# Optimization experiments

Hardware: AMD Instinct MI355X
Metric: run time of the kernel (lower is better)

## Reference

```python
import jax, jax.numpy as jnp
import numpy as np

EPS = 1e-10  # faithful quirk: masked scores are set to eps, NOT -inf
LN_EPS = 1e-5
N_HEADS, D_MODEL, D_HEAD, D_MLP = 16, 1024, 64, 4096
INIT_RANGE = 0.02


def setup_inputs() -> dict:
    key = jax.random.key(0)
    ks = jax.random.split(key, 8)
    B, S = 2, 2048
    inp = {
        'residual': jax.random.normal(ks[0], (B, S, D_MODEL), jnp.float32),
        'W_key': jax.random.normal(ks[1], (N_HEADS, D_MODEL, D_HEAD), jnp.float32) * INIT_RANGE,
        'W_query': jax.random.normal(ks[2], (N_HEADS, D_MODEL, D_HEAD), jnp.float32) * INIT_RANGE,
        'W_values': jax.random.normal(ks[3], (N_HEADS, D_MODEL, D_HEAD), jnp.float32) * INIT_RANGE,
        'W_attn_out': jax.random.normal(ks[4], (N_HEADS, D_HEAD, D_MODEL), jnp.float32) * INIT_RANGE,
        'B_key': jnp.zeros((N_HEADS, D_HEAD), jnp.float32),
        'B_query': jnp.zeros((N_HEADS, D_HEAD), jnp.float32),
        'B_values': jnp.zeros((N_HEADS, D_HEAD), jnp.float32),
        'B_attn_out': jnp.zeros((D_MODEL,), jnp.float32),
        'ln1_w': jnp.ones((D_MODEL,), jnp.float32),
        'ln1_b': jnp.zeros((D_MODEL,), jnp.float32),
        'ln2_w': jnp.ones((D_MODEL,), jnp.float32),
        'ln2_b': jnp.zeros((D_MODEL,), jnp.float32),
        'W_mlp_in': jax.random.normal(ks[5], (D_MODEL, D_MLP), jnp.float32) * INIT_RANGE,
        'W_mlp_out': jax.random.normal(ks[6], (D_MLP, D_MODEL), jnp.float32) * INIT_RANGE,
        'B_mlp_in': jnp.zeros((D_MLP,), jnp.float32),
        'B_mlp_out': jnp.zeros((D_MODEL,), jnp.float32),
    }
    return inp


def _layernorm(x, w, b):
    mean = jnp.mean(x, axis=-1, keepdims=True)
    var = jnp.mean(jnp.square(x - mean), axis=-1, keepdims=True)  # biased var
    return (x - mean) / jnp.sqrt(var + LN_EPS) * w + b


def _attention(x, W_key, W_query, W_values, W_attn_out,
               B_key, B_query, B_values, B_attn_out):
    S = x.shape[1]
    keys = jnp.einsum('bse,neh->bsnh', x, W_key) + B_key
    queries = jnp.einsum('bse,neh->bsnh', x, W_query) + B_query
    values = jnp.einsum('bse,neh->bsnh', x, W_values) + B_values
    scores = jnp.einsum('bknh,bqnh->bnqk', keys, queries) / (D_HEAD ** 0.5)
    # faithful to source: positions where query < key are set to eps (not -inf)
    q_idx = jnp.arange(S)[:, None]
    k_idx = jnp.arange(S)[None, :]
    scores = jnp.where(q_idx < k_idx, EPS, scores)
    probs = jax.nn.softmax(scores, axis=3)
    weighted = jnp.einsum('bnqk,bknh->bqnh', probs, values)
    out = jnp.einsum('bqnh,nhe->bqe', weighted, W_attn_out) + B_attn_out
    return out


def reference(residual, W_key, W_query, W_values, W_attn_out,
              B_key, B_query, B_values, B_attn_out,
              ln1_w, ln1_b, ln2_w, ln2_b,
              W_mlp_in, W_mlp_out, B_mlp_in, B_mlp_out):
    mid = _attention(_layernorm(residual, ln1_w, ln1_b),
                     W_key, W_query, W_values, W_attn_out,
                     B_key, B_query, B_values, B_attn_out) + residual
    h = jnp.einsum('bse,em->bsm', _layernorm(mid, ln2_w, ln2_b), W_mlp_in) + B_mlp_in
    h = jax.nn.gelu(h, approximate=False)  # torch nn.GELU default = exact erf
    out = jnp.einsum('bsm,me->bse', h, W_mlp_out) + B_mlp_out + mid
    return out
```

## Files before the change

### kernel.cpp

```cpp
#include <hip/hip_runtime.h>
#include <hip/hip_bf16.h>


typedef __hip_bfloat16 bf16;
typedef __bf16 bf16x8 __attribute__((ext_vector_type(8)));
typedef float f32x4 __attribute__((ext_vector_type(4)));
typedef unsigned short u16x8 __attribute__((ext_vector_type(8)));
#define DEV static __device__ __forceinline__

DEV float b2f(bf16 v) { return __bfloat162float(v); }
DEV bf16 f2b(float v) { return __float2bfloat16(v); }
DEV unsigned short f2bu(float v) { return __builtin_bit_cast(unsigned short, __float2bfloat16(v)); }
DEV float ldin(const void* p, size_t i, int f32) {
  return f32 ? ((const float*)p)[i] : b2f(((const bf16*)p)[i]);
}
DEV void stout(void* p, size_t i, int f32, float v) {
  if (f32) ((float*)p)[i] = v;
  else     ((bf16*)p)[i] = f2b(v);
}
DEV f32x4 mfma16(bf16x8 a, bf16x8 b, f32x4 c) {
  return __builtin_amdgcn_mfma_f32_16x16x32_bf16(a, b, c, 0, 0, 0);
}
DEV float exp2fast(float x) {
  float r;
  asm volatile("v_exp_f32 %0, %1\n\ts_nop 0" : "=v"(r) : "v"(x));
  return r;
}
DEV void gload16(const void* g, void* l) {
  __builtin_amdgcn_global_load_lds(
      (const __attribute__((address_space(1))) unsigned int*)g,
      (__attribute__((address_space(3))) unsigned int*)l, 16, 0, 0);
}

__global__ void detect_kernel(const void* __restrict__ ln1w, int* __restrict__ flag) {
  if (threadIdx.x == 0 && blockIdx.x == 0) {
    const unsigned short* u = (const unsigned short*)ln1w;
    flag[0] = (u[0] == 0x3F80u) ? 0 : 1;
  }
}

__global__ void pack_bias(const void* __restrict__ Bq, const void* __restrict__ Bk,
                          const void* __restrict__ Bv, const void* __restrict__ Bao,
                          const void* __restrict__ Bmi, const void* __restrict__ Bmo,
                          const int* __restrict__ flagp, float* __restrict__ out) {
  int t = blockIdx.x * 256 + threadIdx.x;
  if (t >= 9216) return;
  int f32 = flagp[0];
  float v;
  if (t < 1024)      v = ldin(Bq, t, f32);
  else if (t < 2048) v = ldin(Bk, t - 1024, f32);
  else if (t < 3072) v = ldin(Bv, t - 2048, f32);
  else if (t < 4096) v = ldin(Bao, t - 3072, f32);
  else if (t < 8192) v = ldin(Bmi, t - 4096, f32);
  else               v = ldin(Bmo, t - 8192, f32);
  out[t] = v;
}

__global__ __launch_bounds__(256) void tsplit(const void* __restrict__ src,
                                              bf16* __restrict__ hi,
                                              const int* __restrict__ flagp,
                                              int K, int N) {
  int i = blockIdx.x * 256 + threadIdx.x;
  int f32 = flagp[0];
  int k = i / N, n = i - k * N;
  float v = ldin(src, i, f32);
  hi[(size_t)n * K + k] = f2b(v);
}

__global__ __launch_bounds__(256) void tsplit_qkv(const void* __restrict__ Wq,
                                                  const void* __restrict__ Wk,
                                                  const void* __restrict__ Wv,
                                                  bf16* __restrict__ hi,
                                                  const int* __restrict__ flagp) {
  int i = blockIdx.x * 256 + threadIdx.x;
  int f32 = flagp[0];
  int sec = i >> 20;
  int rem = i & 1048575;
  int hh = rem >> 16, kr = rem & 65535;
  int k = kr >> 6, d = kr & 63;
  const void* W = (sec == 0) ? Wq : (sec == 1) ? Wk : Wv;
  float v = ldin(W, (size_t)hh * 65536 + (size_t)k * 64 + d, f32);
  int n = sec * 1024 + hh * 64 + d;
  hi[(size_t)n * 1024 + k] = f2b(v);
}

__global__ __launch_bounds__(256) void vsuffix(const bf16* __restrict__ v2,
                                               float* __restrict__ suf) {
  const int head = blockIdx.x >> 6, d = blockIdx.x & 63;
  const int t = threadIdx.x;
  const int T = t >> 3, s0 = (t & 7) * 8;
  const bf16* src = v2 + (size_t)head * 131072 + (size_t)T * 4096 + d * 64 + s0;
  u16x8 u = *(const u16x8*)src;
  float s = 0.f;
#pragma unroll
  for (int j = 0; j < 8; j++) s += b2f(__builtin_bit_cast(bf16, (unsigned short)u[j]));
#pragma unroll
  for (int off = 1; off < 8; off <<= 1) s += __shfl_xor(s, off);
  __shared__ float cs[32];
  if ((t & 7) == 0) cs[T] = s;
  __syncthreads();
  if (t < 33) {
    float acc = 0.f;
    for (int j = t; j < 32; j++) acc += cs[j];
    suf[((size_t)head * 33 + t) * 64 + d] = acc;
  }
}

__global__ __launch_bounds__(256) void ln_kernel(const void* __restrict__ x,
                                                 const void* __restrict__ w,
                                                 const void* __restrict__ bb,
                                                 bf16* __restrict__ out,
                                                 const int* __restrict__ flagp) {
  const int f32 = flagp[0];
  const int row = blockIdx.x, t = threadIdx.x;
  const size_t base = (size_t)row * 1024;
  float v[4];
#pragma unroll
  for (int i = 0; i < 4; i++) v[i] = ldin(x, base + t + 256 * i, f32);
  float s1 = v[0] + v[1] + v[2] + v[3];
  float s2 = v[0] * v[0] + v[1] * v[1] + v[2] * v[2] + v[3] * v[3];
#pragma unroll
  for (int off = 32; off; off >>= 1) {
    s1 += __shfl_xor(s1, off);
    s2 += __shfl_xor(s2, off);
  }
  __shared__ float r1[4], r2[4];
  if ((t & 63) == 0) { r1[t >> 6] = s1; r2[t >> 6] = s2; }
  __syncthreads();
  s1 = r1[0] + r1[1] + r1[2] + r1[3];
  s2 = r2[0] + r2[1] + r2[2] + r2[3];
  float mean = s1 * (1.f / 1024.f);
  float var = s2 * (1.f / 1024.f) - mean * mean;
  float rstd = rsqrtf(var + 1e-5f);
#pragma unroll
  for (int i = 0; i < 4; i++) {
    int idx = t + 256 * i;
    out[base + idx] = f2b((v[i] - mean) * rstd * ldin(w, idx, f32) + ldin(bb, idx, f32));
  }
}

template <int MODE>
__global__ __launch_bounds__(256) void gemm_bt2(const bf16* __restrict__ A,
                                                const bf16* __restrict__ BT,
                                                const float* __restrict__ bias,
                                                const void* extra, void* outp,
                                                const int* __restrict__ flagp,
                                                int N, int K, int nx) {
  __shared__ __align__(16) unsigned short As[128][64];
  __shared__ __align__(16) unsigned short Bs[128][64];
  const int f32 = flagp[0];
  const int t = threadIdx.x;
  const int lane = t & 63, wv = t >> 6;
  const int quad = lane >> 4, l15 = lane & 15;
  const int wm = (wv >> 1) * 64, wn = (wv & 1) * 64;
  const int pB = blockIdx.x, cpx = gridDim.x >> 3;
  const int id = (pB & 7) * cpx + (pB >> 3);
  const int m0 = (id / nx) * 128, n0 = (id % nx) * 128;
  f32x4 acc[4][4] = {};
  const int rl = lane >> 3, G = lane & 7;
  const int sg = (G ^ rl) * 8;
  const int l7 = l15 & 7;
  for (int k0 = 0; k0 < K; k0 += 64) {
#pragma unroll
    for (int c = 0; c < 4; c++) {
      const int ch = wv * 4 + c;
      const int row = ch * 8 + rl;
      gload16(A + (size_t)(m0 + row) * K + k0 + sg, &As[ch * 8][0]);
      gload16(BT + (size_t)(n0 + row) * K + k0 + sg, &Bs[ch * 8][0]);
    }
    __syncthreads();
#pragma unroll
    for (int sub = 0; sub < 2; sub++) {
      const int gsw = (((sub * 4 + quad) ^ l7)) * 8;
      bf16x8 af[4], bh[4];
#pragma unroll
      for (int f = 0; f < 4; f++) {
        af[f] = __builtin_bit_cast(bf16x8, *(const u16x8*)&As[wm + f * 16 + l15][gsw]);
        bh[f] = __builtin_bit_cast(bf16x8, *(const u16x8*)&Bs[wn + f * 16 + l15][gsw]);
      }
#pragma unroll
      for (int fm = 0; fm < 4; fm++)
#pragma unroll
        for (int fn = 0; fn < 4; fn++)
          acc[fm][fn] = mfma16(af[fm], bh[fn], acc[fm][fn]);
    }
    __syncthreads();
  }
  if (MODE == 3) {
    bf16* q2 = (bf16*)outp;
    bf16* k2 = q2 + 4194304;
    bf16* v2 = (bf16*)const_cast<void*>(extra);
#pragma unroll
    for (int fm = 0; fm < 4; fm++) {
      int rowb = m0 + wm + fm * 16 + quad * 4;
      int bq = rowb >> 11, sb = rowb & 2047;
#pragma unroll
      for (int fn = 0; fn < 4; fn++) {
        int col = n0 + wn + fn * 16 + l15;
        float bcol = bias[col];
        int sec = col >> 10;
        int hd = col & 1023;
        size_t hbase = (size_t)(bq * 16 + (hd >> 6)) * 131072;
        int d = hd & 63;
        if (sec == 2) {
          unsigned long long pk = 0;
#pragma unroll
          for (int r = 0; r < 4; r++)
            pk |= (unsigned long long)f2bu(acc[fm][fn][r] + bcol) << (16 * r);
          *(unsigned long long*)&v2[hbase + (size_t)(sb >> 6) * 4096 + d * 64 + (sb & 63)] = pk;
        } else {
          bf16* dst = sec ? k2 : q2;
#pragma unroll
          for (int r = 0; r < 4; r++)
            dst[hbase + (size_t)(sb + r) * 64 + d] = f2b(acc[fm][fn][r] + bcol);
        }
      }
    }
  } else {
#pragma unroll
    for (int fm = 0; fm < 4; fm++) {
#pragma unroll
      for (int r = 0; r < 4; r++) {
        int row = m0 + wm + fm * 16 + quad * 4 + r;
#pragma unroll
        for (int fn = 0; fn < 4; fn++) {
          int col = n0 + wn + fn * 16 + l15;
          float v = acc[fm][fn][r] + bias[col];
          if (MODE == 1) {
            size_t idx = (size_t)row * N + col;
            v += ldin(extra, idx, f32);
            stout(outp, idx, f32, v);
          } else {
            v = 0.5f * v * (1.f + erff(v * 0.70710678118654752f));
            ((bf16*)outp)[(size_t)row * N + col] = f2b(v);
          }
        }
      }
    }
  }
}

__global__ __launch_bounds__(256) void gemm_bt3(const bf16* __restrict__ A,
                                                const bf16* __restrict__ BT,
                                                const float* __restrict__ bias,
                                                const void* extra, void* outp,
                                                const int* __restrict__ flagp,
                                                int N, int K) {
  __shared__ __align__(16) unsigned short As[64][64];
  __shared__ __align__(16) unsigned short Bs[128][64];
  const int f32 = flagp[0];
  const int t = threadIdx.x;
  const int lane = t & 63, wv = t >> 6;
  const int quad = lane >> 4, l15 = lane & 15;
  const int wm = (wv >> 1) * 32, wn = (wv & 1) * 64;
  const int pB = blockIdx.x, cpx = gridDim.x >> 3;
  const int id = (pB & 7) * cpx + (pB >> 3);
  const int m0 = (id >> 3) * 64, n0 = (id & 7) * 128;
  f32x4 acc[2][4] = {};
  const int rl = lane >> 3, G = lane & 7;
  const int sg = (G ^ rl) * 8;
  const int l7 = l15 & 7;
  for (int k0 = 0; k0 < K; k0 += 64) {
#pragma unroll
    for (int c = 0; c < 2; c++) {
      const int ch = wv * 2 + c;
      gload16(A + (size_t)(m0 + ch * 8 + rl) * K + k0 + sg, &As[ch * 8][0]);
    }
#pragma unroll
    for (int c = 0; c < 4; c++) {
      const int ch = wv * 4 + c;
      gload16(BT + (size_t)(n0 + ch * 8 + rl) * K + k0 + sg, &Bs[ch * 8][0]);
    }
    __syncthreads();
#pragma unroll
    for (int sub = 0; sub < 2; sub++) {
      const int gsw = (((sub * 4 + quad) ^ l7)) * 8;
      bf16x8 af[2], bh[4];
#pragma unroll
      for (int f = 0; f < 2; f++)
        af[f] = __builtin_bit_cast(bf16x8, *(const u16x8*)&As[wm + f * 16 + l15][gsw]);
#pragma unroll
      for (int f = 0; f < 4; f++)
        bh[f] = __builtin_bit_cast(bf16x8, *(const u16x8*)&Bs[wn + f * 16 + l15][gsw]);
#pragma unroll
      for (int fm = 0; fm < 2; fm++)
#pragma unroll
        for (int fn = 0; fn < 4; fn++)
          acc[fm][fn] = mfma16(af[fm], bh[fn], acc[fm][fn]);
    }
    __syncthreads();
  }
#pragma unroll
  for (int fm = 0; fm < 2; fm++) {
#pragma unroll
    for (int r = 0; r < 4; r++) {
      int row = m0 + wm + fm * 16 + quad * 4 + r;
#pragma unroll
      for (int fn = 0; fn < 4; fn++) {
        int col = n0 + wn + fn * 16 + l15;
        float v = acc[fm][fn][r] + bias[col];
        size_t idx = (size_t)row * N + col;
        v += ldin(extra, idx, f32);
        stout(outp, idx, f32, v);
      }
    }
  }
}

template <int MODE, int QKV>
__global__ __launch_bounds__(256) void gemm_nn(const bf16* __restrict__ A,
                                               const void* __restrict__ B0,
                                               const void* __restrict__ B1,
                                               const void* __restrict__ B2,
                                               const float* __restrict__ bias,
                                               const void* extra, void* outp,
                                               const int* __restrict__ flagp,
                                               int N, int K, size_t ooff) {
  __shared__ unsigned short As[128][40];
  __shared__ unsigned short Bh[128][40];
  __shared__ unsigned short Bl[128][40];
  const int f32 = flagp[0];
  const int t = threadIdx.x;
  const int lane = t & 63, wv = t >> 6;
  const int quad = lane >> 4, l15 = lane & 15;
  const int wm = (wv >> 1) * 64, wn = (wv & 1) * 64;
  const int m0 = blockIdx.y * 128, n0 = blockIdx.x * 128;
  const void* B = B0;
  if (QKV) B = (n0 < 1024) ? B0 : (n0 < 2048) ? B1 : B2;
  f32x4 acc[4][4] = {};
  const int row_a = t >> 2;
  const int kc = (t & 3) * 8;
  const int cB = t & 127;
  const int e0 = t >> 7;
  for (int k0 = 0; k0 < K; k0 += 32) {
    uint4 a0 = *(const uint4*)(A + (size_t)(m0 + row_a) * K + k0 + kc);
    uint4 a1 = *(const uint4*)(A + (size_t)(m0 + 64 + row_a) * K + k0 + kc);
    *(uint4*)&As[row_a][kc] = a0;
    *(uint4*)&As[64 + row_a][kc] = a1;
#pragma unroll
    for (int rep = 0; rep < 8; rep++) {
      int e = (rep * 2 + e0) * 2;
      size_t a0i, a1i;
      if (QKV) {
        int cs = (n0 + cB) & 1023;
        size_t wb = (size_t)(cs >> 6) * 65536 + (cs & 63);
        a0i = wb + (size_t)(k0 + e) * 64;
        a1i = wb + (size_t)(k0 + e + 1) * 64;
      } else {
        a0i = (size_t)(k0 + e) * N + n0 + cB;
        a1i = a0i + N;
      }
      float v0 = ldin(B, a0i, f32);
      float v1 = ldin(B, a1i, f32);
      unsigned short h0 = f2bu(v0), h1 = f2bu(v1);
      float l0 = v0 - b2f(__builtin_bit_cast(bf16, h0));
      float l1 = v1 - b2f(__builtin_bit_cast(bf16, h1));
      *(unsigned int*)&Bh[cB][e] = (unsigned int)h0 | ((unsigned int)h1 << 16);
      *(unsigned int*)&Bl[cB][e] = (unsigned int)f2bu(l0) | ((unsigned int)f2bu(l1) << 16);
    }
    __syncthreads();
    bf16x8 af[4], bh[4], bl[4];
#pragma unroll
    for (int f = 0; f < 4; f++) {
      af[f] = __builtin_bit_cast(bf16x8, *(const u16x8*)&As[wm + f * 16 + l15][quad * 8]);
      bh[f] = __builtin_bit_cast(bf16x8, *(const u16x8*)&Bh[wn + f * 16 + l15][quad * 8]);
      bl[f] = __builtin_bit_cast(bf16x8, *(const u16x8*)&Bl[wn + f * 16 + l15][quad * 8]);
    }
#pragma unroll
    for (int fm = 0; fm < 4; fm++)
#pragma unroll
      for (int fn = 0; fn < 4; fn++)
        acc[fm][fn] = mfma16(af[fm], bh[fn], acc[fm][fn]);
    if (f32) {
#pragma unroll
      for (int fm = 0; fm < 4; fm++)
#pragma unroll
        for (int fn = 0; fn < 4; fn++)
          acc[fm][fn] = mfma16(af[fm], bl[fn], acc[fm][fn]);
    }
    __syncthreads();
  }
#pragma unroll
  for (int fm = 0; fm < 4; fm++) {
#pragma unroll
    for (int r = 0; r < 4; r++) {
      int row = m0 + wm + fm * 16 + quad * 4 + r;
#pragma unroll
      for (int fn = 0; fn < 4; fn++) {
        int col = n0 + wn + fn * 16 + l15;
        float v = acc[fm][fn][r] + bias[col];
        size_t idx = (size_t)row * N + col;
        if (MODE == 1) {
          v += ldin(extra, ooff + idx, f32);
          stout(outp, ooff + idx, f32, v);
        } else if (MODE == 2) {
          v = 0.5f * v * (1.f + erff(v * 0.70710678118654752f));
          ((bf16*)outp)[idx] = f2b(v);
        } else {
          ((bf16*)outp)[idx] = f2b(v);
        }
      }
    }
  }
}

__global__ __launch_bounds__(256, 2) void attn_split(const bf16* __restrict__ qkv2,
                                                     const float* __restrict__ suf,
                                                     float* __restrict__ part0,
                                                     float* __restrict__ part1,
                                                     float* __restrict__ lp0buf,
                                                     float* __restrict__ lp1buf,
                                                     bf16* __restrict__ weighted) {
  __shared__ __align__(16) unsigned short P[4][4][16][72];
  const int t = threadIdx.x;
  const int lane = t & 63, wv = t >> 6;
  const int quad = lane >> 4, l15 = lane & 15;
  const int w = blockIdx.x * 4 + wv;
  const int g = w & 31;
  const int wi = w >> 5;
  int qc, Tlo, Thi, mode;
  if (wi < 32) {
    qc = 31 - (wi >> 1);
    if ((wi & 1) == 0) { Tlo = 0; Thi = 15; mode = 1; }
    else               { Tlo = 16; Thi = qc; mode = 2; }
  } else {
    qc = 47 - wi; Tlo = 0; Thi = qc; mode = 0;
  }
  const int b = g >> 4, n = g & 15;
  const bf16* Qh = qkv2 + (size_t)g * 131072;
  const bf16* Kh = qkv2 + 4194304 + (size_t)g * 131072;
  const bf16* Vh = qkv2 + 8388608 + (size_t)g * 131072;
  bf16x8 aq[4][2];
#pragma unroll
  for (int qg = 0; qg < 4; qg++) {
    size_t qr = (size_t)(qc * 64 + qg * 16 + l15) * 64;
    aq[qg][0] = __builtin_bit_cast(bf16x8, *(const u16x8*)(Qh + qr + quad * 8));
    aq[qg][1] = __builtin_bit_cast(bf16x8, *(const u16x8*)(Qh + qr + 32 + quad * 8));
  }
  float lp[4][4] = {};
  f32x4 o[4][4] = {};
  const float C = 0.125f * 1.44269504088896f;
  for (int T = Tlo; T <= Thi; ++T) {
    const int kk = T * 64;
    u16x8 uk[4][2];
#pragma unroll
    for (int sub = 0; sub < 4; sub++) {
      size_t kr = (size_t)(kk + sub * 16 + l15) * 64;
      uk[sub][0] = *(const u16x8*)(Kh + kr + quad * 8);
      uk[sub][1] = *(const u16x8*)(Kh + kr + 32 + quad * 8);
    }
    const bf16* Vt = Vh + (size_t)T * 4096;
    u16x8 vu[2][4];
#pragma unroll
    for (int sl = 0; sl < 2; sl++)
#pragma unroll
      for (int f = 0; f < 4; f++)
        vu[sl][f] = *(const u16x8*)(Vt + (size_t)(f * 16 + l15) * 64 + sl * 32 + quad * 8);
#pragma unroll
    for (int qg = 0; qg < 4; qg++) {
      const int qgb = qc * 64 + qg * 16 + quad * 4;
      f32x4 s[4];
      __builtin_amdgcn_s_setprio(1);
#pragma unroll
      for (int sub = 0; sub < 4; sub++) {
        f32x4 sc = {0.f, 0.f, 0.f, 0.f};
        sc = mfma16(aq[qg][0], __builtin_bit_cast(bf16x8, uk[sub][0]), sc);
        sc = mfma16(aq[qg][1], __builtin_bit_cast(bf16x8, uk[sub][1]), sc);
        s[sub] = sc;
      }
      __builtin_amdgcn_s_setprio(0);
#pragma unroll
      for (int sub = 0; sub < 4; sub++) {
#pragma unroll
        for (int r = 0; r < 4; r++) {
          float pv = exp2fast(s[sub][r] * C);
          int kg = kk + sub * 16 + l15;
          pv = (qgb + r < kg) ? 1.0f : pv;
          lp[qg][r] += pv;
          P[wv][qg][quad * 4 + r][l15 + 16 * sub] = f2bu(pv);
        }
      }
      u16x8 pu0 = *(const u16x8*)&P[wv][qg][l15][quad * 8];
      u16x8 pu1 = *(const u16x8*)&P[wv][qg][l15][32 + quad * 8];
      __builtin_amdgcn_s_setprio(1);
#pragma unroll
      for (int f = 0; f < 4; f++) {
        o[qg][f] = mfma16(__builtin_bit_cast(bf16x8, pu0), __builtin_bit_cast(bf16x8, vu[0][f]), o[qg][f]);
        o[qg][f] = mfma16(__builtin_bit_cast(bf16x8, pu1), __builtin_bit_cast(bf16x8, vu[1][f]), o[qg][f]);
      }
      __builtin_amdgcn_s_setprio(0);
    }
  }
  if (mode != 1) {
    const float* sp = suf + ((size_t)g * 33 + (qc + 1)) * 64;
#pragma unroll
    for (int f = 0; f < 4; f++) {
      float sv = sp[f * 16 + l15];
#pragma unroll
      for (int qg = 0; qg < 4; qg++)
#pragma unroll
        for (int r = 0; r < 4; r++) o[qg][f][r] += sv;
    }
  }
#pragma unroll
  for (int off = 8; off; off >>= 1)
#pragma unroll
    for (int qg = 0; qg < 4; qg++)
#pragma unroll
      for (int r = 0; r < 4; r++) lp[qg][r] += __shfl_xor(lp[qg][r], off);
  if (mode == 0) {
    const float mcnt = (float)(2048 - 64 * (qc + 1));
#pragma unroll
    for (int qg = 0; qg < 4; qg++) {
#pragma unroll
      for (int r = 0; r < 4; r++) {
        float inv = 1.f / (lp[qg][r] + mcnt);
        int qg_row = qc * 64 + qg * 16 + quad * 4 + r;
        size_t base = (size_t)(b * 2048 + qg_row) * 1024 + n * 64;
#pragma unroll
        for (int f = 0; f < 4; f++)
          weighted[base + f * 16 + l15] = f2b(o[qg][f][r] * inv);
      }
    }
  } else {
    float* part = (mode == 1) ? part0 : part1;
    float* lpb  = (mode == 1) ? lp0buf : lp1buf;
    size_t pb = (size_t)(g * 16 + (qc - 16)) * 4096;
#pragma unroll
    for (int qg = 0; qg < 4; qg++) {
#pragma unroll
      for (int r = 0; r < 4; r++) {
        int row = qg * 16 + quad * 4 + r;
#pragma unroll
        for (int f = 0; f < 4; f++)
          part[pb + (size_t)row * 64 + f * 16 + l15] = o[qg][f][r];
        if (l15 == 0) lpb[(size_t)(g * 16 + (qc - 16)) * 64 + row] = lp[qg][r];
      }
    }
  }
}

__global__ __launch_bounds__(256) void attn_combine(const float* __restrict__ part0,
                                                    const float* __restrict__ part1,
                                                    const float* __restrict__ lp0,
                                                    const float* __restrict__ lp1,
                                                    bf16* __restrict__ weighted) {
  int i = blockIdx.x * 256 + threadIdx.x;
  int d = i & 63, row = (i >> 6) & 63, qq = (i >> 12) & 15, g = i >> 16;
  int qc = qq + 16;
  size_t pi = ((size_t)(g * 16 + qq) * 64 + row) * 64 + d;
  float o = part0[pi] + part1[pi];
  size_t li = (size_t)(g * 16 + qq) * 64 + row;
  float mcnt = (float)(2048 - 64 * (qc + 1));
  float lp = lp0[li] + lp1[li] + mcnt;
  int b = g >> 4, n = g & 15;
  int qg = qc * 64 + row;
  weighted[(size_t)(b * 2048 + qg) * 1024 + n * 64 + d] = f2b(o / lp);
}

__global__ __launch_bounds__(256) void attn_old(const bf16* __restrict__ qkv,
                                                bf16* __restrict__ weighted) {
  __shared__ unsigned short P[4][16][40];
  const int t = threadIdx.x;
  const int lane = t & 63, wv = t >> 6;
  const int quad = lane >> 4, l15 = lane & 15;
  const int bid = blockIdx.x;
  const int qc = bid & 31, bn = bid >> 5;
  const int b = bn >> 4, n = bn & 15;
  const int q0 = qc * 64 + wv * 16;
  const bf16* Qb = qkv + (size_t)b * 2048 * 3072 + n * 64;
  const bf16* Kb = Qb + 1024;
  const unsigned short* Vus = (const unsigned short*)(Qb + 2048);
  bf16x8 aq0, aq1;
  {
    u16x8 u0 = *(const u16x8*)(Qb + (size_t)(q0 + l15) * 3072 + quad * 8);
    u16x8 u1 = *(const u16x8*)(Qb + (size_t)(q0 + l15) * 3072 + 32 + quad * 8);
    aq0 = __builtin_bit_cast(bf16x8, u0);
    aq1 = __builtin_bit_cast(bf16x8, u1);
  }
  float m_[4] = {-30000.f, -30000.f, -30000.f, -30000.f};
  float l_[4] = {0.f, 0.f, 0.f, 0.f};
  f32x4 o[4] = {};
  for (int kk = 0; kk < 2048; kk += 32) {
    f32x4 s[2];
#pragma unroll
    for (int sub = 0; sub < 2; sub++) {
      int krow = kk + sub * 16 + l15;
      u16x8 uk0 = *(const u16x8*)(Kb + (size_t)krow * 3072 + quad * 8);
      u16x8 uk1 = *(const u16x8*)(Kb + (size_t)krow * 3072 + 32 + quad * 8);
      f32x4 sc = {0.f, 0.f, 0.f, 0.f};
      sc = mfma16(aq0, __builtin_bit_cast(bf16x8, uk0), sc);
      sc = mfma16(aq1, __builtin_bit_cast(bf16x8, uk1), sc);
#pragma unroll
      for (int r = 0; r < 4; r++) {
        int qg = q0 + quad * 4 + r;
        int kg = kk + sub * 16 + l15;
        s[sub][r] = (qg < kg) ? 1e-10f : sc[r] * 0.125f;
      }
    }
    float mr[4];
#pragma unroll
    for (int r = 0; r < 4; r++) mr[r] = fmaxf(s[0][r], s[1][r]);
#pragma unroll
    for (int off = 8; off; off >>= 1)
#pragma unroll
      for (int r = 0; r < 4; r++) mr[r] = fmaxf(mr[r], __shfl_xor(mr[r], off));
    float al[4];
#pragma unroll
    for (int r = 0; r < 4; r++) {
      float mn = fmaxf(m_[r], mr[r]);
      al[r] = __expf(m_[r] - mn);
      m_[r] = mn;
    }
    f32x4 p0, p1;
    float rs[4];
#pragma unroll
    for (int r = 0; r < 4; r++) {
      p0[r] = __expf(s[0][r] - m_[r]);
      p1[r] = __expf(s[1][r] - m_[r]);
      rs[r] = p0[r] + p1[r];
    }
#pragma unroll
    for (int off = 8; off; off >>= 1)
#pragma unroll
      for (int r = 0; r < 4; r++) rs[r] += __shfl_xor(rs[r], off);
#pragma unroll
    for (int r = 0; r < 4; r++) l_[r] = l_[r] * al[r] + rs[r];
#pragma unroll
    for (int f = 0; f < 4; f++)
#pragma unroll
      for (int r = 0; r < 4; r++) o[f][r] *= al[r];
#pragma unroll
    for (int r = 0; r < 4; r++) {
      P[wv][quad * 4 + r][l15] = f2bu(p0[r]);
      P[wv][quad * 4 + r][16 + l15] = f2bu(p1[r]);
    }
    __syncthreads();
    u16x8 pu = *(const u16x8*)&P[wv][l15][quad * 8];
    bf16x8 pf = __builtin_bit_cast(bf16x8, pu);
#pragma unroll
    for (int f = 0; f < 4; f++) {
      u16x8 vu;
#pragma unroll
      for (int j = 0; j < 8; j++)
        vu[j] = Vus[(size_t)(kk + quad * 8 + j) * 3072 + f * 16 + l15];
      o[f] = mfma16(pf, __builtin_bit_cast(bf16x8, vu), o[f]);
    }
    __syncthreads();
  }
#pragma unroll
  for (int r = 0; r < 4; r++) {
    float inv = 1.f / l_[r];
    int qg = q0 + quad * 4 + r;
    size_t base = (size_t)(b * 2048 + qg) * 1024 + n * 64;
#pragma unroll
    for (int f = 0; f < 4; f++)
      weighted[base + f * 16 + l15] = f2b(o[f][r] * inv);
  }
}

extern "C" void kernel_launch(void* const* d_in, const int* in_sizes, int n_in,
                              void* d_out, int out_size, void* d_ws, size_t ws_size,
                              hipStream_t stream) {
  const void* residual = d_in[0];
  const void* W_key    = d_in[1];
  const void* W_query  = d_in[2];
  const void* W_values = d_in[3];
  const void* W_ao     = d_in[4];
  const void* B_key    = d_in[5];
  const void* B_query  = d_in[6];
  const void* B_values = d_in[7];
  const void* B_ao     = d_in[8];
  const void* ln1w     = d_in[9];
  const void* ln1b     = d_in[10];
  const void* ln2w     = d_in[11];
  const void* ln2b     = d_in[12];
  const void* W_mi     = d_in[13];
  const void* W_mo     = d_in[14];
  const void* B_mi     = d_in[15];
  const void* B_mo     = d_in[16];

  char* ws = (char*)d_ws;
  float* biasA  = (float*)ws;
  int*   flag   = (int*)(ws + 36864);
  bf16*  slotA  = (bf16*)(ws + 40960);
  bf16*  xn = slotA, *wtd = slotA, *xn2 = slotA;

  detect_kernel<<<1, 64, 0, stream>>>(ln1w, flag);
  pack_bias<<<36, 256, 0, stream>>>(B_query, B_key, B_values, B_ao, B_mi, B_mo,
                                    flag, biasA);

  if (ws_size >= (size_t)83927040) {
    bf16*  qkv2    = (bf16*)(ws + 8429568);
    bf16*  q2      = qkv2;
    bf16*  v2      = qkv2 + 8388608;
    bf16*  h       = (bf16*)(ws + 8429568);
    bf16*  qkvT_hi = (bf16*)(ws + 33595392);
    float* suf     = (float*)(ws + 39886848);
    float* lp0buf  = (float*)(ws + 40157184);
    float* lp1buf  = (float*)(ws + 40288256);
    bf16*  aoT_hi  = (bf16*)(ws + 46178304);
    bf16*  miT_hi  = (bf16*)(ws + 50372608);
    float* part0   = (float*)(ws + 58761216);
    bf16*  moT_hi  = (bf16*)(ws + 67149824);
    float* part1   = (float*)(ws + 75538432);

    tsplit_qkv<<<12288, 256, 0, stream>>>(W_query, W_key, W_values, qkvT_hi, flag);
    tsplit<<<4096, 256, 0, stream>>>(W_ao, aoT_hi, flag, 1024, 1024);
    tsplit<<<16384, 256, 0, stream>>>(W_mi, miT_hi, flag, 1024, 4096);
    tsplit<<<16384, 256, 0, stream>>>(W_mo, moT_hi, flag, 4096, 1024);

    ln_kernel<<<4096, 256, 0, stream>>>(residual, ln1w, ln1b, xn, flag);
    gemm_bt2<3><<<768, 256, 0, stream>>>(xn, qkvT_hi, biasA,
                                         v2, q2, flag, 3072, 1024, 24);
    vsuffix<<<2048, 256, 0, stream>>>(v2, suf);
    attn_split<<<384, 256, 0, stream>>>(qkv2, suf, part0, part1,
                                        lp0buf, lp1buf, wtd);
    attn_combine<<<8192, 256, 0, stream>>>(part0, part1, lp0buf, lp1buf, wtd);
    gemm_bt3<<<512, 256, 0, stream>>>(wtd, aoT_hi, biasA + 3072,
                                      residual, d_out, flag, 1024, 1024);
    ln_kernel<<<4096, 256, 0, stream>>>(d_out, ln2w, ln2b, xn2, flag);
    gemm_bt2<2><<<1024, 256, 0, stream>>>(xn2, miT_hi, biasA + 4096,
                                          nullptr, h, flag, 4096, 1024, 32);
    gemm_bt3<<<512, 256, 0, stream>>>(h, moT_hi, biasA + 8192,
                                      d_out, d_out, flag, 1024, 4096);
  } else {
    bf16* qkv   = (bf16*)(ws + 8429568);
    bf16* hhalf = (bf16*)(ws + 16818176);

    ln_kernel<<<4096, 256, 0, stream>>>(residual, ln1w, ln1b, xn, flag);
    gemm_nn<0, 1><<<dim3(24, 32), 256, 0, stream>>>(xn, W_query, W_key, W_values,
                                                    biasA, nullptr, qkv, flag,
                                                    3072, 1024, 0);
    attn_old<<<1024, 256, 0, stream>>>(qkv, wtd);
    gemm_nn<1, 0><<<dim3(8, 32), 256, 0, stream>>>(wtd, W_ao, nullptr, nullptr,
                                                   biasA + 3072, residual, d_out,
                                                   flag, 1024, 1024, 0);
    ln_kernel<<<4096, 256, 0, stream>>>(d_out, ln2w, ln2b, xn2, flag);
    for (int half = 0; half < 2; ++half) {
      const bf16* a2 = xn2 + (size_t)half * 2048 * 1024;
      size_t ooff = (size_t)half * 2048 * 1024;
      gemm_nn<2, 0><<<dim3(32, 16), 256, 0, stream>>>(a2, W_mi, nullptr, nullptr,
                                                      biasA + 4096, nullptr, hhalf,
                                                      flag, 4096, 1024, 0);
      gemm_nn<1, 0><<<dim3(8, 16), 256, 0, stream>>>(hhalf, W_mo, nullptr, nullptr,
                                                     biasA + 8192, d_out, d_out,
                                                     flag, 1024, 4096, ooff);
    }
  }
}
```

Baseline: 459.8 us.

## Split attention key loop across wave pairs and use polynomial erf in GELU

The attention kernel now assigns each work item to a pair of waves that take alternating key tiles. The second wave writes its partial output and row sums to shared memory, and the first wave merges them before the existing epilogue. The grid doubles to 768 blocks. This is meant to cut the serial per-wave key loop and raise parallelism, at the cost of about 35 KB of extra LDS per block (which may limit the two-blocks-per-CU target), a block-wide barrier, and idle waves when the tile count is odd. Separately, GELU's erff is replaced with an Abramowitz-Stegun polynomial using a hardware reciprocal and exp2, which is cheaper but less precise.

```diff
diff --git a/kernel.cpp b/kernel.cpp
--- a/kernel.cpp
+++ b/kernel.cpp
@@ -25,6 +25,18 @@
   float r;
   asm volatile("v_exp_f32 %0, %1\n\ts_nop 0" : "=v"(r) : "v"(x));
   return r;
+}
+DEV float fasterf(float x) {
+  float ax = __builtin_fabsf(x);
+  float t = __builtin_amdgcn_rcpf(__builtin_fmaf(0.3275911f, ax, 1.f));
+  float p = __builtin_fmaf(t, 1.061405429f, -1.453152027f);
+  p = __builtin_fmaf(t, p, 1.421413741f);
+  p = __builtin_fmaf(t, p, -0.284496736f);
+  p = __builtin_fmaf(t, p, 0.254829592f);
+  p = p * t;
+  float e = exp2fast(ax * ax * -1.44269504088896f);
+  float r = 1.f - p * e;
+  return x < 0.f ? -r : r;
 }
 DEV void gload16(const void* g, void* l) {
   __builtin_amdgcn_global_load_lds(
@@ -231,7 +243,7 @@
             v += ldin(extra, idx, f32);
             stout(outp, idx, f32, v);
           } else {
-            v = 0.5f * v * (1.f + erff(v * 0.70710678118654752f));
+            v = 0.5f * v * (1.f + fasterf(v * 0.70710678118654752f));
             ((bf16*)outp)[(size_t)row * N + col] = f2b(v);
           }
         }
@@ -412,12 +424,15 @@
                                                      float* __restrict__ lp1buf,
                                                      bf16* __restrict__ weighted) {
   __shared__ __align__(16) unsigned short P[4][4][16][72];
+  __shared__ float xo[2][64][68];
+  __shared__ float xlp[2][64];
   const int t = threadIdx.x;
   const int lane = t & 63, wv = t >> 6;
   const int quad = lane >> 4, l15 = lane & 15;
-  const int w = blockIdx.x * 4 + wv;
-  const int g = w & 31;
-  const int wi = w >> 5;
+  const int pair = wv >> 1, half = wv & 1;
+  const int iw = blockIdx.x * 2 + pair;
+  const int g = iw & 31;
+  const int wi = iw >> 5;
   int qc, Tlo, Thi, mode;
   if (wi < 32) {
     qc = 31 - (wi >> 1);
@@ -440,7 +455,7 @@
   float lp[4][4] = {};
   f32x4 o[4][4] = {};
   const float C = 0.125f * 1.44269504088896f;
-  for (int T = Tlo; T <= Thi; ++T) {
+  for (int T = Tlo + half; T <= Thi; T += 2) {
     const int kk = T * 64;
     u16x8 uk[4][2];
 #pragma unroll
@@ -491,6 +506,36 @@
       __builtin_amdgcn_s_setprio(0);
     }
   }
+#pragma unroll
+  for (int off = 8; off; off >>= 1)
+#pragma unroll
+    for (int qg = 0; qg < 4; qg++)
+#pragma unroll
+      for (int r = 0; r < 4; r++) lp[qg][r] += __shfl_xor(lp[qg][r], off);
+  if (half == 1) {
+#pragma unroll
+    for (int qg = 0; qg < 4; qg++) {
+#pragma unroll
+      for (int r = 0; r < 4; r++) {
+        int row = qg * 16 + quad * 4 + r;
+#pragma unroll
+        for (int f = 0; f < 4; f++) xo[pair][row][f * 16 + l15] = o[qg][f][r];
+        if (l15 == 0) xlp[pair][row] = lp[qg][r];
+      }
+    }
+  }
+  __syncthreads();
+  if (half == 1) return;
+#pragma unroll
+  for (int qg = 0; qg < 4; qg++) {
+#pragma unroll
+    for (int r = 0; r < 4; r++) {
+      int row = qg * 16 + quad * 4 + r;
+#pragma unroll
+      for (int f = 0; f < 4; f++) o[qg][f][r] += xo[pair][row][f * 16 + l15];
+      lp[qg][r] += xlp[pair][row];
+    }
+  }
   if (mode != 1) {
     const float* sp = suf + ((size_t)g * 33 + (qc + 1)) * 64;
 #pragma unroll
@@ -502,12 +547,6 @@
         for (int r = 0; r < 4; r++) o[qg][f][r] += sv;
     }
   }
-#pragma unroll
-  for (int off = 8; off; off >>= 1)
-#pragma unroll
-    for (int qg = 0; qg < 4; qg++)
-#pragma unroll
-      for (int r = 0; r < 4; r++) lp[qg][r] += __shfl_xor(lp[qg][r], off);
   if (mode == 0) {
     const float mcnt = (float)(2048 - 64 * (qc + 1));
 #pragma unroll
@@ -714,7 +753,7 @@
     gemm_bt2<3><<<768, 256, 0, stream>>>(xn, qkvT_hi, biasA,
                                          v2, q2, flag, 3072, 1024, 24);
     vsuffix<<<2048, 256, 0, stream>>>(v2, suf);
-    attn_split<<<384, 256, 0, stream>>>(qkv2, suf, part0, part1,
+    attn_split<<<768, 256, 0, stream>>>(qkv2, suf, part0, part1,
                                         lp0buf, lp1buf, wtd);
     attn_combine<<<8192, 256, 0, stream>>>(part0, part1, lp0buf, lp1buf, wtd);
     gemm_bt3<<<512, 256, 0, stream>>>(wtd, aoT_hi, biasA + 3072,
```

Result: faster. 449.2 us (-2.3%).
